# Optimization experiments

Measured on AMD Instinct MI355X. Metric: run time of the kernel, lower is better.

The kernel has to match this reference:

```python
import jax, jax.numpy as jnp
import numpy as np

jax.config.update("jax_enable_x64", True)

N = 16          # particles per jet
B = 32          # number of jets
L2 = 1e-4       # qpth_l2_strength ('L2' form: Q = L2*I, p = flattened distance matrix)
ITERS = 20      # fixed interior-point iterations (converges well past solver tolerance)
SIGMA = 0.1     # centering parameter


def _build_G(n):
    # Inequality matrix, same layout as the torch code: G = [-I ; marginal-row-sums ; marginal-col-sums]
    m = n * n
    G1 = -np.eye(m)
    G2 = np.zeros((2 * n, m))
    for i in range(n):
        G2[i, i * n:(i + 1) * n] = 1.0      # sum_j x_{ij} <= w1_i
    for j in range(n):
        G2[n + j, j::n] = 1.0               # sum_i x_{ij} <= w2_j
    return jnp.asarray(np.concatenate([G1, G2], axis=0))  # [m + 2n, m]


def _solve_qp(p, h, b, G):
    """Batched infeasible-start primal-dual interior point solver for
    min 0.5*L2*||x||^2 + p.x  s.t.  G x <= h,  1.x = b  (same QP qpth solves)."""
    Bn, m = p.shape
    nin = G.shape[0]
    ones_m = jnp.ones((m,), p.dtype)
    x = jnp.zeros((Bn, m), p.dtype)
    s = jnp.ones((Bn, nin), p.dtype)
    z = jnp.ones((Bn, nin), p.dtype)
    y = jnp.zeros((Bn,), p.dtype)
    eye_m = jnp.eye(m, dtype=p.dtype)

    def step(carry, _):
        x, s, z, y = carry
        mu = jnp.mean(s * z, axis=1)                    # [B]
        rx = L2 * x + p + z @ G + y[:, None]            # dual residual   (A^T y = y * 1)
        rp = x @ G.T + s - h                            # primal ineq residual
        ra = x.sum(1) - b                               # primal eq residual
        rs = s * z - SIGMA * mu[:, None]                # complementarity residual
        d = z / s
        # H = Q + G^T diag(d) G  -> [B, m, m]
        H = L2 * eye_m + jnp.einsum('rk,br,rl->bkl', G, d, G)
        r1 = rx + ((z * rp - rs) / s) @ G
        Lc = jnp.linalg.cholesky(H)

        def chosolve(rhs):  # rhs [B, m] -> H^{-1} rhs
            t = jax.scipy.linalg.solve_triangular(Lc, rhs[..., None], lower=True)
            return jax.scipy.linalg.solve_triangular(Lc, t, lower=True, trans='T')[..., 0]

        u = chosolve(r1)
        v = chosolve(jnp.broadcast_to(ones_m, (Bn, m)))
        dy = (ra - u.sum(1)) / v.sum(1)                 # Schur complement on the 1-row equality
        dx = -u - v * dy[:, None]
        ds = -rp - dx @ G.T
        dz = (-rs - z * ds) / s
        # fraction-to-boundary step
        ds_safe = jnp.where(ds < 0, ds, -jnp.ones_like(ds))
        dz_safe = jnp.where(dz < 0, dz, -jnp.ones_like(dz))
        a_s = jnp.min(jnp.where(ds < 0, -s / ds_safe, jnp.inf), axis=1)
        a_z = jnp.min(jnp.where(dz < 0, -z / dz_safe, jnp.inf), axis=1)
        alpha = 0.99 * jnp.minimum(1.0, jnp.minimum(a_s, a_z))[:, None]
        x = x + alpha * dx
        s = s + alpha * ds
        z = z + alpha * dz
        y = y + alpha[:, 0] * dy
        return (x, s, z, y), None

    (x, s, z, y), _ = jax.lax.scan(step, (x, s, z, y), None, length=ITERS)
    return x


def setup_inputs() -> dict:
    key = jax.random.key(0)
    k1, k2 = jax.random.split(key)
    jets1 = jax.random.uniform(k1, (B, N, 3), dtype=jnp.float32)
    jets2 = jax.random.uniform(k2, (B, N, 3), dtype=jnp.float32)
    return {"jets1": jets1, "jets2": jets2}


def reference(jets1, jets2):
    j1 = jets1.astype(jnp.float64)
    j2 = jets2.astype(jnp.float64)
    nb, n = j1.shape[0], j1.shape[1]
    # pairwise (eta, phi) distances, same sign/epsilon as the torch code
    diffs = -(j1[:, :, None, :2] - j2[:, None, :, :2]) + 1e-12   # [B, n, n, 2]
    dists = jnp.sqrt(jnp.sum(diffs * diffs, axis=3))             # [B, n, n]
    w1 = j1[:, :, 2]
    w2 = j2[:, :, 2]
    p = dists.reshape(nb, n * n)
    h = jnp.concatenate([jnp.zeros((nb, n * n), p.dtype), w1, w2], axis=1)
    b = jnp.minimum(w1.sum(1), w2.sum(1))
    G = _build_G(n)
    flow = _solve_qp(p, h, b, G)                                  # [B, n*n]
    energy_diff = jnp.abs(w1.sum(1) - w2.sum(1))
    emds = jnp.sum(p * flow, axis=1) + energy_diff                # [B]
    return emds
```

## Files before the change

### kernel.cpp

```cpp
#include <hip/hip_runtime.h>
#include <math.h>

#define L2C  1e-4
#define SIGC 0.1
#define NITER 20

__device__ __forceinline__ double rld(double v, int lane) {
    union { double d; int i[2]; } u, r; u.d = v;
    r.i[0] = __builtin_amdgcn_readlane(u.i[0], lane);
    r.i[1] = __builtin_amdgcn_readlane(u.i[1], lane);
    return r.d;
}
template <int CTRL>
__device__ __forceinline__ double dppd(double v) {
    union { double d; int i[2]; } u, r; u.d = v;
    r.i[0] = __builtin_amdgcn_update_dpp(0, u.i[0], CTRL, 0xF, 0xF, true);
    r.i[1] = __builtin_amdgcn_update_dpp(0, u.i[1], CTRL, 0xF, 0xF, true);
    return r.d;
}
__device__ __forceinline__ double sum16d(double v) {
    v += dppd<0xB1>(v); v += dppd<0x4E>(v); v += dppd<0x124>(v); v += dppd<0x128>(v);
    return v;
}
__device__ __forceinline__ double cross4d(double v) {
    v += __shfl_xor(v, 16, 64); v += __shfl_xor(v, 32, 64); return v;
}
template <int CTRL>
__device__ __forceinline__ float dppf(float v) {
    return __int_as_float(__builtin_amdgcn_update_dpp(0, __float_as_int(v), CTRL, 0xF, 0xF, true));
}
__device__ __forceinline__ float min16f(float v) {
    v = fminf(v, dppf<0xB1>(v)); v = fminf(v, dppf<0x4E>(v));
    v = fminf(v, dppf<0x124>(v)); v = fminf(v, dppf<0x128>(v));
    return v;
}
__device__ __forceinline__ float cross4minf(float v) {
    v = fminf(v, __shfl_xor(v, 16, 64)); v = fminf(v, __shfl_xor(v, 32, 64)); return v;
}
__device__ __forceinline__ double drcp(double d) {
    double x = (double)__builtin_amdgcn_rcpf((float)d);
    x = x * (2.0 - d * x);
    return x;
}
__device__ __forceinline__ float frcpf(float x) { return __builtin_amdgcn_rcpf(x); }

__global__ __launch_bounds__(64, 1) void emd_ip_kernel(const float* __restrict__ jets1,
                                                       const float* __restrict__ jets2,
                                                       float* __restrict__ out) {
    const int l = threadIdx.x;
    const int b = blockIdx.x;
    const int q = l & 15;
    const int r = l >> 4;

    __shared__ double invDl[16 * 17];
    __shared__ double Sst[16 * 17];
    __shared__ double Lst[16 * 17];
    __shared__ double GstR[16], GstI[16];
    __shared__ double QstR[16], QstI[16];

    const float* p1 = jets1 + b * 48;
    const float* p2 = jets2 + b * 48;

    double ax = (double)p1[3 * q], ay = (double)p1[3 * q + 1];
    double px[4];
#pragma unroll
    for (int c = 0; c < 4; c++) {
        int j = 4 * c + r;
        double d0 = ((double)p2[3 * j]     - ax) + 1e-12;
        double d1 = ((double)p2[3 * j + 1] - ay) + 1e-12;
        px[c] = sqrt(d0 * d0 + d1 * d1);
    }
    double h_rt = (double)p1[3 * q + 2];
    double h_ct[4];
#pragma unroll
    for (int c = 0; c < 4; c++) h_ct[c] = (double)p2[3 * (4 * c + r) + 2];

    double sw1 = sum16d(h_rt);
    double sw2 = sum16d((double)p2[3 * q + 2]);
    const double sB = fmin(sw1, sw2);
    const double sE = fabs(sw1 - sw2);

    double x[4] = {0, 0, 0, 0}, s[4] = {1, 1, 1, 1}, z[4] = {1, 1, 1, 1};
    double yv = 0.0;
    double s_rt = 1.0, z_rt = 1.0;
    double s_ct[4] = {1, 1, 1, 1}, z_ct[4] = {1, 1, 1, 1};
    double rsx = 0.0;
    double cs[4] = {0, 0, 0, 0};
    double ra = -sB;

    for (int it = 0; it < NITER; ++it) {
        double mub = s[0]*z[0] + s[1]*z[1] + s[2]*z[2] + s[3]*z[3]
                   + 0.25 * (s_rt * z_rt)
                   + 0.0625 * (s_ct[0]*z_ct[0] + s_ct[1]*z_ct[1] + s_ct[2]*z_ct[2] + s_ct[3]*z_ct[3]);
        double mu = sum16d(cross4d(mub)) * (1.0 / 288.0);
        if (!(mu >= 1e-4)) break;
        double sgmu = SIGC * mu;

        double is_rt = drcp(s_rt);
        double rp_rt = rsx + s_rt - h_rt;
        double rs_rt = s_rt * z_rt - sgmu;
        double tt_rt = (z_rt * (rsx - h_rt) + sgmu) * is_rt;
        double is_ct[4], rp_ct[4], rs_ct[4], tt_ct[4];
#pragma unroll
        for (int c = 0; c < 4; c++) {
            is_ct[c] = drcp(s_ct[c]);
            rp_ct[c] = cs[c] + s_ct[c] - h_ct[c];
            rs_ct[c] = s_ct[c] * z_ct[c] - sgmu;
            tt_ct[c] = (z_ct[c] * (cs[c] - h_ct[c]) + sgmu) * is_ct[c];
        }

        double rp[4], rs[4], iD[4], r1[4], rD1[4], is_[4];
#pragma unroll
        for (int c = 0; c < 4; c++) {
            is_[c] = drcp(s[c]);
            double rx = L2C * x[c] + px[c] + (-z[c] + z_rt + z_ct[c]) + yv;
            rp[c] = s[c] - x[c];
            rs[c] = s[c] * z[c] - sgmu;
            double tk = (sgmu - z[c] * x[c]) * is_[c];
            iD[c] = drcp(L2C + z[c] * is_[c]);
            r1[c] = rx - tk + tt_rt + tt_ct[c];
            rD1[c] = r1[c] * iD[c];
            invDl[q * 17 + 4 * c + r] = iD[c];
        }

        double rsI = cross4d(iD[0] + iD[1] + iD[2] + iD[3]);
        double rsR = cross4d(rD1[0] + rD1[1] + rD1[2] + rD1[3]);
        double csI[4], csR[4];
#pragma unroll
        for (int c = 0; c < 4; c++) { csI[c] = sum16d(iD[c]); csR[c] = sum16d(rD1[c]); }

        double ar = drcp(s_rt * drcp(z_rt) + rsI);
        double aR = ar * rsR;
        double aI = ar * rsI;

        double gpR[4], gpI[4], bb[4];
#pragma unroll
        for (int c = 0; c < 4; c++) {
            gpR[c] = csR[c] - sum16d(aR * iD[c]);
            gpI[c] = csI[c] - sum16d(aI * iD[c]);
            bb[c]  = s_ct[c] * drcp(z_ct[c]) + csI[c];
            if (q == 4 * c + r) { GstR[q] = gpR[c]; GstI[q] = gpI[c]; }
        }

        double accS[4] = {0, 0, 0, 0};
#pragma unroll
        for (int t = 0; t < 16; t++) {
            double w = rld(ar, t) * invDl[t * 17 + q];
#pragma unroll
            for (int c = 0; c < 4; c++) accS[c] += w * invDl[t * 17 + 4 * c + r];
        }
#pragma unroll
        for (int c = 0; c < 4; c++)
            Sst[q * 17 + 4 * c + r] = ((q == 4 * c + r) ? bb[c] : 0.0) - accS[c];

        double Sr[16];
#pragma unroll
        for (int j2 = 0; j2 < 16; j2++) Sr[j2] = Sst[q * 17 + j2];
        double D0own = Sr[q];

        double invdv = 0.0;
#pragma unroll
        for (int kk = 0; kk < 16; kk++) {
            double flo = fmax(1e-12 * fabs(rld(D0own, kk)), 1e-280);
            double dkk = fmax(rld(Sr[kk], kk), flo);
            double inv = drcp(dkk);
            invdv = (q == kk) ? inv : invdv;
            double Lc = Sr[kk] * inv;
            if (l < 16) Lst[kk * 17 + l] = Lc;
#pragma unroll
            for (int jj = kk + 1; jj < 16; jj++)
                Sr[jj] -= Sr[kk] * rld(Lc, jj);
            Sr[kk] = Lc;
        }

        double y1 = GstR[q], y2 = GstI[q];
        double LTr[16];
#pragma unroll
        for (int kk = 0; kk < 16; kk++) LTr[kk] = Lst[q * 17 + kk];

#pragma unroll
        for (int kk = 0; kk < 16; kk++) {
            double t1 = rld(y1, kk);
            double t2 = rld(y2, kk);
            if (q > kk) { y1 -= Sr[kk] * t1; y2 -= Sr[kk] * t2; }
        }
        y1 *= invdv;
        y2 *= invdv;
#pragma unroll
        for (int kk = 15; kk >= 0; kk--) {
            double t1 = rld(y1, kk);
            double t2 = rld(y2, kk);
            if (q < kk) { y1 -= LTr[kk] * t1; y2 -= LTr[kk] * t2; }
        }

        if (l < 16) { QstR[l] = y1; QstI[l] = y2; }
        double qc1c[4], qcvc[4];
#pragma unroll
        for (int c = 0; c < 4; c++) { qc1c[c] = QstR[4 * c + r]; qcvc[c] = QstI[4 * c + r]; }

        double pr1 = iD[0]*qc1c[0] + iD[1]*qc1c[1] + iD[2]*qc1c[2] + iD[3]*qc1c[3];
        double prv = iD[0]*qcvc[0] + iD[1]*qcvc[1] + iD[2]*qcvc[2] + iD[3]*qcvc[3];
        double qr1 = ar * (rsR - cross4d(pr1));
        double qrv = ar * (rsI - cross4d(prv));

        double u[4], v[4];
#pragma unroll
        for (int c = 0; c < 4; c++) {
            u[c] = (r1[c] - qr1 - qc1c[c]) * iD[c];
            v[c] = (1.0  - qrv - qcvc[c]) * iD[c];
        }
        double usum = sum16d(cross4d(u[0] + u[1] + u[2] + u[3]));
        double vsum = sum16d(cross4d(v[0] + v[1] + v[2] + v[3]));
        double dy = (ra - usum) * drcp(vsum);

        double dx[4];
#pragma unroll
        for (int c = 0; c < 4; c++) dx[c] = -u[c] - v[c] * dy;
        double rsdx = cross4d(dx[0] + dx[1] + dx[2] + dx[3]);
        double csdx[4];
#pragma unroll
        for (int c = 0; c < 4; c++) csdx[c] = sum16d(dx[c]);
        double sumdx = -usum - vsum * dy;

        float amP = 1e30f, amD = 1e30f;
        double ds[4], dz[4];
#pragma unroll
        for (int c = 0; c < 4; c++) {
            ds[c] = dx[c] - rp[c];
            dz[c] = -(rs[c] + z[c] * ds[c]) * is_[c];
            if (ds[c] < 0.0) amP = fminf(amP, (float)s[c] * frcpf((float)(-ds[c])));
            if (dz[c] < 0.0) amD = fminf(amD, (float)z[c] * frcpf((float)(-dz[c])));
        }
        double ds_rt = -rp_rt - rsdx;
        double dz_rt = -(rs_rt + z_rt * ds_rt) * is_rt;
        if (ds_rt < 0.0) amP = fminf(amP, (float)s_rt * frcpf((float)(-ds_rt)));
        if (dz_rt < 0.0) amD = fminf(amD, (float)z_rt * frcpf((float)(-dz_rt)));
        double ds_ct[4], dz_ct[4];
#pragma unroll
        for (int c = 0; c < 4; c++) {
            ds_ct[c] = -rp_ct[c] - csdx[c];
            dz_ct[c] = -(rs_ct[c] + z_ct[c] * ds_ct[c]) * is_ct[c];
            if (ds_ct[c] < 0.0) amP = fminf(amP, (float)s_ct[c] * frcpf((float)(-ds_ct[c])));
            if (dz_ct[c] < 0.0) amD = fminf(amD, (float)z_ct[c] * frcpf((float)(-dz_ct[c])));
        }
        float aPf = min16f(cross4minf(amP));
        float aDf = min16f(cross4minf(amD));
        double alphaP = 0.99 * fmin(1.0, (double)aPf);
        double alphaD = 0.99 * fmin(1.0, (double)aDf);
        bool good = ((dy - dy) == 0.0);
        alphaP = good ? alphaP : 0.0;
        alphaD = good ? alphaD : 0.0;

#pragma unroll
        for (int c = 0; c < 4; c++) {
            x[c] += alphaP * dx[c];
            s[c] += alphaP * ds[c];
            z[c] += alphaD * dz[c];
            s_ct[c] += alphaP * ds_ct[c];
            z_ct[c] += alphaD * dz_ct[c];
            cs[c] += alphaP * csdx[c];
        }
        yv += alphaD * dy;
        s_rt += alphaP * ds_rt;
        z_rt += alphaD * dz_rt;
        rsx += alphaP * rsdx;
        ra  += alphaP * sumdx;
    }

    double e = sum16d(cross4d(px[0]*x[0] + px[1]*x[1] + px[2]*x[2] + px[3]*x[3]));
    if (l == 0) out[b] = (float)(e + sE);
}

extern "C" void kernel_launch(void* const* d_in, const int* in_sizes, int n_in,
                              void* d_out, int out_size, void* d_ws, size_t ws_size,
                              hipStream_t stream) {
    const float* jets1 = (const float*)d_in[0];
    const float* jets2 = (const float*)d_in[1];
    float* out = (float*)d_out;
    int B = in_sizes[0] / 48;
    emd_ip_kernel<<<dim3(B), dim3(64), 0, stream>>>(jets1, jets2, out);
}
```

Before: 116.3 us.

## Use permlane swaps for cross-row reductions and trim LDS round trips

Cross-row reductions now use permlane16/32 swap builtins when the compiler provides them, instead of ds_bpermute shuffles. The Q vector is broadcast with __shfl instead of a shared-memory round trip. The reciprocal computations are hoisted above the mu reduction so they can overlap it, and the Cholesky pivot floors are precomputed outside the serial elimination loop. All of this is meant to shorten the latency-bound per-iteration critical path in a single-wavefront kernel. The permlane path depends on builtin availability and on swap semantics being correct for the reduction.

Measured after the change: 115.5 us. Within noise of the previous version (-0.7%).

```diff
diff --git a/kernel.cpp b/kernel.cpp
--- a/kernel.cpp
+++ b/kernel.cpp
@@ -4,6 +4,15 @@
 #define L2C  1e-4
 #define SIGC 0.1
 #define NITER 20
+
+#if defined(__has_builtin)
+#  if __has_builtin(__builtin_amdgcn_permlane16_swap) && __has_builtin(__builtin_amdgcn_permlane32_swap)
+#    define HAVE_PLSWAP 1
+#  endif
+#endif
+#ifndef HAVE_PLSWAP
+#  define HAVE_PLSWAP 0
+#endif
 
 __device__ __forceinline__ double rld(double v, int lane) {
     union { double d; int i[2]; } u, r; u.d = v;
@@ -22,9 +31,6 @@
     v += dppd<0xB1>(v); v += dppd<0x4E>(v); v += dppd<0x124>(v); v += dppd<0x128>(v);
     return v;
 }
-__device__ __forceinline__ double cross4d(double v) {
-    v += __shfl_xor(v, 16, 64); v += __shfl_xor(v, 32, 64); return v;
-}
 template <int CTRL>
 __device__ __forceinline__ float dppf(float v) {
     return __int_as_float(__builtin_amdgcn_update_dpp(0, __float_as_int(v), CTRL, 0xF, 0xF, true));
@@ -34,8 +40,35 @@
     v = fminf(v, dppf<0x124>(v)); v = fminf(v, dppf<0x128>(v));
     return v;
 }
+__device__ __forceinline__ double mkd(unsigned lo, unsigned hi) {
+    union { unsigned u[2]; double d; } r; r.u[0] = lo; r.u[1] = hi; return r.d;
+}
+__device__ __forceinline__ void dsplit(double v, unsigned &lo, unsigned &hi) {
+    union { double d; unsigned u[2]; } x; x.d = v; lo = x.u[0]; hi = x.u[1];
+}
+__device__ __forceinline__ double cross4d(double v) {
+#if HAVE_PLSWAP
+    unsigned lo, hi; dsplit(v, lo, hi);
+    auto rl = __builtin_amdgcn_permlane16_swap(lo, lo, false, false);
+    auto rh = __builtin_amdgcn_permlane16_swap(hi, hi, false, false);
+    v = mkd(rl[0], rh[0]) + mkd(rl[1], rh[1]);
+    dsplit(v, lo, hi);
+    auto sl = __builtin_amdgcn_permlane32_swap(lo, lo, false, false);
+    auto sh = __builtin_amdgcn_permlane32_swap(hi, hi, false, false);
+    return mkd(sl[0], sh[0]) + mkd(sl[1], sh[1]);
+#else
+    v += __shfl_xor(v, 16, 64); v += __shfl_xor(v, 32, 64); return v;
+#endif
+}
 __device__ __forceinline__ float cross4minf(float v) {
+#if HAVE_PLSWAP
+    auto a = __builtin_amdgcn_permlane16_swap(__float_as_uint(v), __float_as_uint(v), false, false);
+    v = fminf(__uint_as_float(a[0]), __uint_as_float(a[1]));
+    auto b = __builtin_amdgcn_permlane32_swap(__float_as_uint(v), __float_as_uint(v), false, false);
+    return fminf(__uint_as_float(b[0]), __uint_as_float(b[1]));
+#else
     v = fminf(v, __shfl_xor(v, 16, 64)); v = fminf(v, __shfl_xor(v, 32, 64)); return v;
+#endif
 }
 __device__ __forceinline__ double drcp(double d) {
     double x = (double)__builtin_amdgcn_rcpf((float)d);
@@ -56,7 +89,6 @@
     __shared__ double Sst[16 * 17];
     __shared__ double Lst[16 * 17];
     __shared__ double GstR[16], GstI[16];
-    __shared__ double QstR[16], QstI[16];
 
     const float* p1 = jets1 + b * 48;
     const float* p2 = jets2 + b * 48;
@@ -89,6 +121,18 @@
     double ra = -sB;
 
     for (int it = 0; it < NITER; ++it) {
+        double is_rt = drcp(s_rt);
+        double is_ct[4];
+#pragma unroll
+        for (int c = 0; c < 4; c++) is_ct[c] = drcp(s_ct[c]);
+        double is_[4], iD[4];
+#pragma unroll
+        for (int c = 0; c < 4; c++) {
+            is_[c] = drcp(s[c]);
+            iD[c] = drcp(L2C + z[c] * is_[c]);
+            invDl[q * 17 + 4 * c + r] = iD[c];
+        }
+
         double mub = s[0]*z[0] + s[1]*z[1] + s[2]*z[2] + s[3]*z[3]
                    + 0.25 * (s_rt * z_rt)
                    + 0.0625 * (s_ct[0]*z_ct[0] + s_ct[1]*z_ct[1] + s_ct[2]*z_ct[2] + s_ct[3]*z_ct[3]);
@@ -96,31 +140,26 @@
         if (!(mu >= 1e-4)) break;
         double sgmu = SIGC * mu;
 
-        double is_rt = drcp(s_rt);
         double rp_rt = rsx + s_rt - h_rt;
         double rs_rt = s_rt * z_rt - sgmu;
         double tt_rt = (z_rt * (rsx - h_rt) + sgmu) * is_rt;
-        double is_ct[4], rp_ct[4], rs_ct[4], tt_ct[4];
-#pragma unroll
-        for (int c = 0; c < 4; c++) {
-            is_ct[c] = drcp(s_ct[c]);
+        double rp_ct[4], rs_ct[4], tt_ct[4];
+#pragma unroll
+        for (int c = 0; c < 4; c++) {
             rp_ct[c] = cs[c] + s_ct[c] - h_ct[c];
             rs_ct[c] = s_ct[c] * z_ct[c] - sgmu;
             tt_ct[c] = (z_ct[c] * (cs[c] - h_ct[c]) + sgmu) * is_ct[c];
         }
 
-        double rp[4], rs[4], iD[4], r1[4], rD1[4], is_[4];
-#pragma unroll
-        for (int c = 0; c < 4; c++) {
-            is_[c] = drcp(s[c]);
+        double rp[4], rs[4], r1[4], rD1[4];
+#pragma unroll
+        for (int c = 0; c < 4; c++) {
             double rx = L2C * x[c] + px[c] + (-z[c] + z_rt + z_ct[c]) + yv;
             rp[c] = s[c] - x[c];
             rs[c] = s[c] * z[c] - sgmu;
             double tk = (sgmu - z[c] * x[c]) * is_[c];
-            iD[c] = drcp(L2C + z[c] * is_[c]);
             r1[c] = rx - tk + tt_rt + tt_ct[c];
             rD1[c] = r1[c] * iD[c];
-            invDl[q * 17 + 4 * c + r] = iD[c];
         }
 
         double rsI = cross4d(iD[0] + iD[1] + iD[2] + iD[3]);
@@ -156,13 +195,16 @@
         double Sr[16];
 #pragma unroll
         for (int j2 = 0; j2 < 16; j2++) Sr[j2] = Sst[q * 17 + j2];
-        double D0own = Sr[q];
+
+        double flo[16];
+#pragma unroll
+        for (int kk = 0; kk < 16; kk++)
+            flo[kk] = fmax(1e-12 * fabs(rld(Sr[kk], kk)), 1e-280);
 
         double invdv = 0.0;
 #pragma unroll
         for (int kk = 0; kk < 16; kk++) {
-            double flo = fmax(1e-12 * fabs(rld(D0own, kk)), 1e-280);
-            double dkk = fmax(rld(Sr[kk], kk), flo);
+            double dkk = fmax(rld(Sr[kk], kk), flo[kk]);
             double inv = drcp(dkk);
             invdv = (q == kk) ? inv : invdv;
             double Lc = Sr[kk] * inv;
@@ -193,10 +235,12 @@
             if (q < kk) { y1 -= LTr[kk] * t1; y2 -= LTr[kk] * t2; }
         }
 
-        if (l < 16) { QstR[l] = y1; QstI[l] = y2; }
         double qc1c[4], qcvc[4];
 #pragma unroll
-        for (int c = 0; c < 4; c++) { qc1c[c] = QstR[4 * c + r]; qcvc[c] = QstI[4 * c + r]; }
+        for (int c = 0; c < 4; c++) {
+            qc1c[c] = __shfl(y1, 4 * c + r, 64);
+            qcvc[c] = __shfl(y2, 4 * c + r, 64);
+        }
 
         double pr1 = iD[0]*qc1c[0] + iD[1]*qc1c[1] + iD[2]*qc1c[2] + iD[3]*qc1c[3];
         double prv = iD[0]*qcvc[0] + iD[1]*qcvc[1] + iD[2]*qcvc[2] + iD[3]*qcvc[3];
```
